# Kernel tuning notes

Hardware: AMD Instinct MI355X
Metric: run time of the kernel (lower is better)

The kernel has to match this reference:

```python
import jax, jax.numpy as jnp
import numpy as np

N, D, H, L = 100000, 128, 4, 2
C = D // H  # per-head channels
E = 1600000
NEG_SLOPE = 0.2
LN_EPS = 1e-5


def setup_inputs() -> dict:
    key = jax.random.key(0)
    ks = jax.random.split(key, 8)
    x = jax.random.normal(ks[0], (N, D), dtype=jnp.float32)
    edge_index = jax.random.randint(ks[1], (2, E), 0, N, dtype=jnp.int64)
    s = 1.0 / np.sqrt(D)
    Wl = jax.random.normal(ks[2], (L, D, D), dtype=jnp.float32) * s
    Wr = jax.random.normal(ks[3], (L, D, D), dtype=jnp.float32) * s
    att = jax.random.normal(ks[4], (L, H, C), dtype=jnp.float32) * (1.0 / np.sqrt(C))
    bias = jnp.zeros((L, D), dtype=jnp.float32)
    gamma = jnp.ones((L, D), dtype=jnp.float32)
    beta = jnp.zeros((L, D), dtype=jnp.float32)
    return {"x": x, "edge_index": edge_index, "Wl": Wl, "Wr": Wr,
            "att": att, "bias": bias, "gamma": gamma, "beta": beta}


def _gatv2_layer(h, src, dst, Wl, Wr, att, bias):
    # h: (N, D); src/dst: (E2,) with self-loops already appended
    xl = (h @ Wl).reshape(N, H, C)  # source-side transform
    xr = (h @ Wr).reshape(N, H, C)  # target-side transform
    e = jax.nn.leaky_relu(xl[src] + xr[dst], NEG_SLOPE)      # (E2, H, C)
    alpha = jnp.einsum('ehc,hc->eh', e, att)                 # (E2, H)
    # segment softmax over incoming edges of each destination node
    m = jax.ops.segment_max(alpha, dst, num_segments=N)      # (N, H)
    ea = jnp.exp(alpha - m[dst])
    s = jax.ops.segment_sum(ea, dst, num_segments=N)         # (N, H)
    a = ea / s[dst]                                          # (E2, H)
    out = jax.ops.segment_sum(a[:, :, None] * xl[src], dst, num_segments=N)
    return out.reshape(N, D) + bias


def _layer_norm(y, gamma, beta):
    mu = jnp.mean(y, axis=-1, keepdims=True)
    var = jnp.var(y, axis=-1, keepdims=True)
    return (y - mu) * jax.lax.rsqrt(var + LN_EPS) * gamma + beta


def reference(x, edge_index, Wl, Wr, att, bias, gamma, beta):
    # PyG GATv2Conv defaults: add_self_loops=True (eval mode: dropouts identity)
    loops = jnp.arange(N, dtype=edge_index.dtype)
    src = jnp.concatenate([edge_index[0], loops])
    dst = jnp.concatenate([edge_index[1], loops])
    h = x
    for l in range(L):
        g = _gatv2_layer(h, src, dst, Wl[l], Wr[l], att[l], bias[l])
        h = h + jax.nn.elu(_layer_norm(g, gamma[l], beta[l]))
    return h
```

## Files before the change

### kernel.cpp

```cpp
#include <hip/hip_runtime.h>
#include <hip/hip_fp16.h>
#include <math.h>

#define N_NODES 100000
#define D_FEAT  128
#define E_EDGES 1600000
#define E2      (E_EDGES + N_NODES)
#define NEG_SLOPE 0.2f
#define LN_EPS    1e-5f

#define NB   391
#define TS   8192
#define NTIL ((E2 + TS - 1) / TS)

typedef __attribute__((ext_vector_type(4))) float floatx4;
typedef _Float16 h2 __attribute__((ext_vector_type(2)));
typedef _Float16 h8 __attribute__((ext_vector_type(8)));

static __device__ __forceinline__ float fdot2f(h2 a, h2 b, float c) {
#if __has_builtin(__builtin_amdgcn_fdot2)
    return __builtin_amdgcn_fdot2(a, b, c, false);
#else
    return (float)a[0] * (float)b[0] + (float)a[1] * (float)b[1] + c;
#endif
}

static __device__ __forceinline__ h2 shfl_xor_h2(h2 v, int off) {
    int i = __builtin_bit_cast(int, v);
    i = __shfl_xor(i, off);
    return __builtin_bit_cast(h2, i);
}

__global__ __launch_bounds__(1024) void tile_count(const int* __restrict__ edge_dst,
                                                   int* __restrict__ tcnt) {
    __shared__ int h[NB];
    const int t = threadIdx.x;
    if (t < NB) h[t] = 0;
    __syncthreads();
    const int base = blockIdx.x * TS;
#pragma unroll
    for (int j = 0; j < TS / 1024; ++j) {
        int i = base + j * 1024 + t;
        if (i < E2) {
            int d = (i < E_EDGES) ? edge_dst[i] : (i - E_EDGES);
            atomicAdd(&h[d >> 8], 1);
        }
    }
    __syncthreads();
    if (t < NB) tcnt[blockIdx.x * NB + t] = h[t];
}

__global__ __launch_bounds__(256) void col_scan(const int* __restrict__ tcnt,
                                                int* __restrict__ toff,
                                                int* __restrict__ bcnt) {
    __shared__ int s[256];
    const int b = blockIdx.x;
    const int t = threadIdx.x;
    int v = (t < NTIL) ? tcnt[t * NB + b] : 0;
    s[t] = v;
    __syncthreads();
    for (int off = 1; off < 256; off <<= 1) {
        int x = (t >= off) ? s[t - off] : 0;
        __syncthreads();
        s[t] += x;
        __syncthreads();
    }
    if (t < NTIL) toff[t * NB + b] = s[t] - v;
    if (t == 255) bcnt[b] = s[255];
}

__global__ __launch_bounds__(512) void bucket_scan(const int* __restrict__ bcnt,
                                                   int* __restrict__ bstart,
                                                   int* __restrict__ rowstart) {
    __shared__ int s[512];
    const int t = threadIdx.x;
    int v = (t < NB) ? bcnt[t] : 0;
    s[t] = v;
    __syncthreads();
    for (int off = 1; off < 512; off <<= 1) {
        int x = (t >= off) ? s[t - off] : 0;
        __syncthreads();
        s[t] += x;
        __syncthreads();
    }
    if (t <= NB) bstart[t] = s[t] - v;
    if (t == 0) rowstart[N_NODES] = E2;
}

__global__ __launch_bounds__(1024) void tile_scatter(const int* __restrict__ edge_src,
                                                     const int* __restrict__ edge_dst,
                                                     const int* __restrict__ bstart,
                                                     const int* __restrict__ toff,
                                                     unsigned* __restrict__ pairbuf) {
    __shared__ int base[NB];
    __shared__ int cur[NB];
    const int t = threadIdx.x;
    if (t < NB) { base[t] = bstart[t] + toff[blockIdx.x * NB + t]; cur[t] = 0; }
    __syncthreads();
    const int tb = blockIdx.x * TS;
#pragma unroll
    for (int j = 0; j < TS / 1024; ++j) {
        int i = tb + j * 1024 + t;
        if (i < E2) {
            int d, sr;
            if (i < E_EDGES) { d = edge_dst[i]; sr = edge_src[i]; }
            else             { d = i - E_EDGES; sr = d; }
            int b = d >> 8;
            int rank = atomicAdd(&cur[b], 1);
            pairbuf[base[b] + rank] = (unsigned)sr | ((unsigned)(d & 255) << 17);
        }
    }
}

__global__ __launch_bounds__(1024) void bucketize(const unsigned* __restrict__ pairbuf,
                                                  const int* __restrict__ bstart,
                                                  int* __restrict__ rowstart,
                                                  int* __restrict__ csr_src) {
    __shared__ int cnt[256], sc[256], cur[256];
    const int blk = blockIdx.x;
    const int t = threadIdx.x;
    const int nbase = blk << 8;
    if (t < 256) cnt[t] = 0;
    __syncthreads();
    const int e0 = bstart[blk], e1 = bstart[blk + 1];
    for (int p = e0 + t; p < e1; p += 1024)
        atomicAdd(&cnt[pairbuf[p] >> 17], 1);
    __syncthreads();
    int v = (t < 256) ? cnt[t] : 0;
    if (t < 256) sc[t] = v;
    __syncthreads();
    for (int off = 1; off < 256; off <<= 1) {
        int x = (t < 256 && t >= off) ? sc[t - off] : 0;
        __syncthreads();
        if (t < 256) sc[t] += x;
        __syncthreads();
    }
    if (t < 256) {
        int excl = sc[t] - v;
        int node = nbase + t;
        if (node < N_NODES) rowstart[node] = e0 + excl;
        cur[t] = e0 + excl;
    }
    __syncthreads();
    for (int p = e0 + t; p < e1; p += 1024) {
        unsigned pr = pairbuf[p];
        int pos = atomicAdd(&cur[pr >> 17], 1);
        csr_src[pos] = (int)(pr & 0x1FFFF);
    }
}

__global__ void prep_wt(const float* __restrict__ Wl, const float* __restrict__ Wr,
                        const float* __restrict__ att,
                        _Float16* __restrict__ Wt, _Float16* __restrict__ atth) {
    int idx = blockIdx.x * 256 + threadIdx.x;
    if (idx < 65536) {
        int l    = idx >> 15;
        int rem  = idx & 32767;
        int side = rem >> 14;
        int cw   = rem & 16383;
        int col  = cw >> 7, k = cw & 127;
        const float* W = side ? Wr : Wl;
        Wt[idx] = (_Float16)W[l * 16384 + k * 128 + col];
    } else if (idx < 65536 + 256) {
        int j = idx - 65536;
        atth[j] = (_Float16)att[j];
    }
}

__global__ __launch_bounds__(256) void gemm_mfma3(
        const _Float16* __restrict__ hA,
        const float* __restrict__ Afp,
        const _Float16* __restrict__ Wt,
        _Float16* __restrict__ xl, _Float16* __restrict__ xr, int n_rows) {
    const int wave = threadIdx.x >> 6;
    const int lane = threadIdx.x & 63;
    const int m = lane & 15;
    const int q = lane >> 4;
    const int r0 = (blockIdx.x * 4 + wave) * 32;

    int arow0 = r0 + m;        if (arow0 >= n_rows) arow0 = n_rows - 1;
    int arow1 = r0 + 16 + m;   if (arow1 >= n_rows) arow1 = n_rows - 1;

    floatx4 acc[2][2][8];
#pragma unroll
    for (int s = 0; s < 2; ++s)
#pragma unroll
        for (int rt = 0; rt < 2; ++rt)
#pragma unroll
            for (int ct = 0; ct < 8; ++ct) acc[s][rt][ct] = (floatx4){0.f,0.f,0.f,0.f};

#pragma unroll
    for (int ks = 0; ks < 4; ++ks) {
        const int k0 = ks * 32 + q * 8;
        h8 a0, a1;
        if (Afp) {
            float4 f0 = *(const float4*)(Afp + (size_t)arow0 * 128 + k0);
            float4 f1 = *(const float4*)(Afp + (size_t)arow0 * 128 + k0 + 4);
            float4 g0 = *(const float4*)(Afp + (size_t)arow1 * 128 + k0);
            float4 g1 = *(const float4*)(Afp + (size_t)arow1 * 128 + k0 + 4);
            a0 = (h8){(_Float16)f0.x, (_Float16)f0.y, (_Float16)f0.z, (_Float16)f0.w,
                      (_Float16)f1.x, (_Float16)f1.y, (_Float16)f1.z, (_Float16)f1.w};
            a1 = (h8){(_Float16)g0.x, (_Float16)g0.y, (_Float16)g0.z, (_Float16)g0.w,
                      (_Float16)g1.x, (_Float16)g1.y, (_Float16)g1.z, (_Float16)g1.w};
        } else {
            a0 = *(const h8*)(hA + (size_t)arow0 * 128 + k0);
            a1 = *(const h8*)(hA + (size_t)arow1 * 128 + k0);
        }
#pragma unroll
        for (int s = 0; s < 2; ++s) {
#pragma unroll
            for (int ct = 0; ct < 8; ++ct) {
                h8 b = *(const h8*)(Wt + (size_t)s * 16384
                                    + (size_t)(ct * 16 + m) * 128 + k0);
                acc[s][0][ct] = __builtin_amdgcn_mfma_f32_16x16x32_f16(a0, b, acc[s][0][ct], 0, 0, 0);
                acc[s][1][ct] = __builtin_amdgcn_mfma_f32_16x16x32_f16(a1, b, acc[s][1][ct], 0, 0, 0);
            }
        }
    }

#pragma unroll
    for (int s = 0; s < 2; ++s) {
        _Float16* out = s ? xr : xl;
#pragma unroll
        for (int rt = 0; rt < 2; ++rt)
#pragma unroll
            for (int ct = 0; ct < 8; ++ct)
#pragma unroll
                for (int i = 0; i < 4; ++i) {
                    int row = r0 + rt * 16 + q * 4 + i;
                    if (row < n_rows)
                        out[(size_t)row * 128 + ct * 16 + m] = (_Float16)acc[s][rt][ct][i];
                }
    }
}

union U16 { uint4 u; h2 h[4]; };

__global__ __launch_bounds__(256) void gat_node10(
        const _Float16* __restrict__ xl,
        const _Float16* __restrict__ xr,
        const float* __restrict__ h_in_f32,
        const _Float16* __restrict__ h_in_f16,
        const int* __restrict__ rowstart, const int* __restrict__ csr_src,
        const _Float16* __restrict__ atth, const float* __restrict__ bias,
        const float* __restrict__ gamma, const float* __restrict__ beta,
        float* __restrict__ out_f32,
        _Float16* __restrict__ out_f16) {
    const int wave = threadIdx.x >> 6;
    const int lane = threadIdx.x & 63;
    const int node = blockIdx.x * 4 + wave;
    const int esub = lane >> 3;
    const int r    = lane & 7;
    const int c0   = r * 16;
    const int c    = c0 + 2 * esub;

    const int p0 = rowstart[node], p1 = rowstart[node + 1];
    const int pe = p1 - 1;

    U16 xra, xrb, ata, atb;
    {
        const uint4* xp = (const uint4*)(xr + (size_t)node * 128 + c0);
        xra.u = xp[0]; xrb.u = xp[1];
        const uint4* ap = (const uint4*)(atth + c0);
        ata.u = ap[0]; atb.u = ap[1];
    }
    const float2 bi = *(const float2*)(bias + c);
    const h2 ns2 = {(_Float16)NEG_SLOPE, (_Float16)NEG_SLOPE};

    const unsigned short* xls = (const unsigned short*)xl;

    float s = 0.f;
    h2 acc2[8];
#pragma unroll
    for (int j = 0; j < 8; ++j) acc2[j] = (h2){(_Float16)0.f, (_Float16)0.f};

    auto consume = [&](const U16& u0, const U16& u1, bool v) {
        float da = 0.f, db = 0.f;
#pragma unroll
        for (int qq = 0; qq < 4; ++qq) {
            h2 z  = u0.h[qq] + xra.h[qq];
            h2 lk = __builtin_elementwise_max(z, z * ns2);
            da = fdot2f(lk, ata.h[qq], da);
        }
#pragma unroll
        for (int qq = 0; qq < 4; ++qq) {
            h2 z  = u1.h[qq] + xrb.h[qq];
            h2 lk = __builtin_elementwise_max(z, z * ns2);
            db = fdot2f(lk, atb.h[qq], db);
        }
        float d = da + db;
        float alpha = d + __shfl_xor(d, 1);
        float w = v ? __expf(alpha) : 0.f;
        s += w;
        h2 w2 = {(_Float16)w, (_Float16)w};
#pragma unroll
        for (int qq = 0; qq < 4; ++qq)
            acc2[qq] = w2 * u0.h[qq] + acc2[qq];
#pragma unroll
        for (int qq = 0; qq < 4; ++qq)
            acc2[qq + 4] = w2 * u1.h[qq] + acc2[qq + 4];
    };

    int pA = p0 + esub;        if (pA > pe) pA = pe;
    int pB = p0 + 8 + esub;    if (pB > pe) pB = pe;
    int pC = p0 + 16 + esub;   if (pC > pe) pC = pe;
    int i0 = csr_src[pA];
    int i1 = csr_src[pB];
    int i2 = csr_src[pC];

    U16 s0a, s0b, s1a, s1b, s2a, s2b;
    { const uint4* rp = (const uint4*)(xls + (size_t)i0 * 128 + c0); s0a.u = rp[0]; s0b.u = rp[1]; }
    { const uint4* rp = (const uint4*)(xls + (size_t)i1 * 128 + c0); s1a.u = rp[0]; s1b.u = rp[1]; }

    int pb = p0;
    for (;;) {
        {
            int pn = pb + 24 + esub; if (pn > pe) pn = pe;
            int inew = csr_src[pn];
            if (pb + 16 < p1) {
                const uint4* rp = (const uint4*)(xls + (size_t)i2 * 128 + c0);
                s2a.u = rp[0]; s2b.u = rp[1];
            }
            consume(s0a, s0b, (pb + esub) < p1);
            i0 = inew;
            pb += 8; if (pb >= p1) break;
        }
        {
            int pn = pb + 24 + esub; if (pn > pe) pn = pe;
            int inew = csr_src[pn];
            if (pb + 16 < p1) {
                const uint4* rp = (const uint4*)(xls + (size_t)i0 * 128 + c0);
                s0a.u = rp[0]; s0b.u = rp[1];
            }
            consume(s1a, s1b, (pb + esub) < p1);
            i1 = inew;
            pb += 8; if (pb >= p1) break;
        }
        {
            int pn = pb + 24 + esub; if (pn > pe) pn = pe;
            int inew = csr_src[pn];
            if (pb + 16 < p1) {
                const uint4* rp = (const uint4*)(xls + (size_t)i1 * 128 + c0);
                s1a.u = rp[0]; s1b.u = rp[1];
            }
            consume(s2a, s2b, (pb + esub) < p1);
            i2 = inew;
            pb += 8; if (pb >= p1) break;
        }
    }

    float ssum = s;
    ssum += __shfl_xor(ssum, 8);
    ssum += __shfl_xor(ssum, 16);
    ssum += __shfl_xor(ssum, 32);

    const bool sel0 = (esub & 1) != 0;
    const bool sel1 = ((esub >> 1) & 1) != 0;
    const bool sel2 = ((esub >> 2) & 1) != 0;
    h2 b4[4];
#pragma unroll
    for (int k = 0; k < 4; ++k) {
        h2 keep = sel0 ? acc2[2 * k + 1] : acc2[2 * k];
        h2 send = sel0 ? acc2[2 * k]     : acc2[2 * k + 1];
        b4[k] = keep + shfl_xor_h2(send, 8);
    }
    h2 c2[2];
#pragma unroll
    for (int k = 0; k < 2; ++k) {
        h2 keep = sel1 ? b4[2 * k + 1] : b4[2 * k];
        h2 send = sel1 ? b4[2 * k]     : b4[2 * k + 1];
        c2[k] = keep + shfl_xor_h2(send, 16);
    }
    h2 keepf = sel2 ? c2[1] : c2[0];
    h2 sendf = sel2 ? c2[0] : c2[1];
    h2 tot = keepf + shfl_xor_h2(sendf, 32);

    const float invS = 1.f / ssum;
    float g0 = (float)tot[0] * invS + bi.x;
    float g1 = (float)tot[1] * invS + bi.y;

    const float2 ga = *(const float2*)(gamma + c);
    const float2 be = *(const float2*)(beta + c);
    float hx, hy;
    if (h_in_f16) {
        h2 hv = *(const h2*)(h_in_f16 + (size_t)node * 128 + c);
        hx = (float)hv[0]; hy = (float)hv[1];
    } else {
        float2 hv = *(const float2*)(h_in_f32 + (size_t)node * 128 + c);
        hx = hv.x; hy = hv.y;
    }

    float sum = g0 + g1, sq = g0 * g0 + g1 * g1;
#pragma unroll
    for (int off = 1; off < 64; off <<= 1) {
        sum += __shfl_xor(sum, off);
        sq  += __shfl_xor(sq, off);
    }
    float mu   = sum * (1.f / 128.f);
    float var  = sq * (1.f / 128.f) - mu * mu;
    float rstd = rsqrtf(var + LN_EPS);
    float y0 = (g0 - mu) * rstd * ga.x + be.x;
    float y1 = (g1 - mu) * rstd * ga.y + be.y;
    float e0 = (y0 > 0.f) ? y0 : (__expf(y0) - 1.f);
    float e1 = (y1 > 0.f) ? y1 : (__expf(y1) - 1.f);

    float ox = hx + e0;
    float oy = hy + e1;
    if (out_f32) {
        float2 o; o.x = ox; o.y = oy;
        *(float2*)(out_f32 + (size_t)node * 128 + c) = o;
    } else {
        h2 po = {(_Float16)ox, (_Float16)oy};
        *(h2*)(out_f16 + (size_t)node * 128 + c) = po;
    }
}

extern "C" void kernel_launch(void* const* d_in, const int* in_sizes, int n_in,
                              void* d_out, int out_size, void* d_ws, size_t ws_size,
                              hipStream_t stream) {
    const float* x     = (const float*)d_in[0];
    const int*   eidx  = (const int*)d_in[1];
    const float* Wl    = (const float*)d_in[2];
    const float* Wr    = (const float*)d_in[3];
    const float* att   = (const float*)d_in[4];
    const float* bias  = (const float*)d_in[5];
    const float* gamma = (const float*)d_in[6];
    const float* beta  = (const float*)d_in[7];
    float* out = (float*)d_out;

    char* ws = (char*)d_ws;
    _Float16* xl = (_Float16*)ws;              ws += (size_t)N_NODES * 128 * 2;
    _Float16* xr = (_Float16*)ws;              ws += (size_t)N_NODES * 128 * 2;
    _Float16* h16 = (_Float16*)ws;             ws += (size_t)N_NODES * 128 * 2;
    _Float16* Wt  = (_Float16*)ws;             ws += (size_t)65536 * 2;
    _Float16* atth = (_Float16*)ws;            ws += 256 * 2;
    unsigned* pairbuf = (unsigned*)ws;         ws += (size_t)E2 * 4;
    int* tcnt     = (int*)ws; ws += (size_t)NTIL * NB * 4;
    int* toff     = (int*)ws; ws += (size_t)NTIL * NB * 4;
    int* bcnt     = (int*)ws; ws += (NB + 1) * 4;
    int* bstart   = (int*)ws; ws += (NB + 1) * 4;
    int* rowstart = (int*)ws; ws += (size_t)(N_NODES + 4) * 4;
    int* csr_src  = (int*)ws; ws += (size_t)E2 * 4;

    const int* edge_src = eidx;
    const int* edge_dst = eidx + E_EDGES;

    prep_wt<<<257, 256, 0, stream>>>(Wl, Wr, att, Wt, atth);

    tile_count<<<NTIL, 1024, 0, stream>>>(edge_dst, tcnt);
    col_scan<<<NB, 256, 0, stream>>>(tcnt, toff, bcnt);
    bucket_scan<<<1, 512, 0, stream>>>(bcnt, bstart, rowstart);
    tile_scatter<<<NTIL, 1024, 0, stream>>>(edge_src, edge_dst, bstart, toff, pairbuf);
    bucketize<<<NB, 1024, 0, stream>>>(pairbuf, bstart, rowstart, csr_src);

    const int gemm_gx = (N_NODES + 127) / 128;
    for (int l = 0; l < 2; ++l) {
        gemm_mfma3<<<gemm_gx, 256, 0, stream>>>(
            (l == 0) ? nullptr : h16, (l == 0) ? x : nullptr,
            Wt + (size_t)l * 32768, xl, xr, N_NODES);
        gat_node10<<<N_NODES / 4, 256, 0, stream>>>(
            xl, xr,
            (l == 0) ? x : nullptr, (l == 0) ? nullptr : h16,
            rowstart, csr_src,
            atth + l * 128, bias + l * 128, gamma + l * 128, beta + l * 128,
            (l == 1) ? out : nullptr, (l == 0) ? h16 : nullptr);
    }
}
```

Baseline: 388.1 us.

## Replace two-level bucketed CSR build with global-atomic degree count and scatter

Replaces the tiled two-pass bucket sort (per-tile LDS histograms, column scans, pair buffer, per-bucket local sort) with a simple CSR build: global atomic degree count, a three-kernel prefix scan, and a scatter using per-node atomic cursors. This removes the intermediate pair buffer and its extra pass over the edges. In exchange it relies on 1.7M global atomics to random addresses, twice, and the order of edges within each row becomes nondeterministic.

```diff
diff --git a/kernel.cpp b/kernel.cpp
--- a/kernel.cpp
+++ b/kernel.cpp
@@ -9,10 +9,6 @@
 #define NEG_SLOPE 0.2f
 #define LN_EPS    1e-5f
 
-#define NB   391
-#define TS   8192
-#define NTIL ((E2 + TS - 1) / TS)
-
 typedef __attribute__((ext_vector_type(4))) float floatx4;
 typedef _Float16 h2 __attribute__((ext_vector_type(2)));
 typedef _Float16 h8 __attribute__((ext_vector_type(8)));
@@ -31,121 +27,81 @@
     return __builtin_bit_cast(h2, i);
 }
 
-__global__ __launch_bounds__(1024) void tile_count(const int* __restrict__ edge_dst,
-                                                   int* __restrict__ tcnt) {
-    __shared__ int h[NB];
+__global__ __launch_bounds__(1024) void zero_deg(int* __restrict__ deg) {
+    int i = blockIdx.x * 1024 + threadIdx.x;
+    if (i < N_NODES) deg[i] = 0;
+}
+
+__global__ __launch_bounds__(256) void count_deg(const int* __restrict__ edge_dst,
+                                                 int* __restrict__ deg) {
+    int i = blockIdx.x * 256 + threadIdx.x;
+    if (i < E2) {
+        int d = (i < E_EDGES) ? edge_dst[i] : (i - E_EDGES);
+        atomicAdd(&deg[d], 1);
+    }
+}
+
+__global__ __launch_bounds__(1024) void scan1(const int* __restrict__ deg,
+                                              int* __restrict__ rowstart,
+                                              int* __restrict__ btot) {
+    __shared__ int s[1024];
     const int t = threadIdx.x;
-    if (t < NB) h[t] = 0;
-    __syncthreads();
-    const int base = blockIdx.x * TS;
-#pragma unroll
-    for (int j = 0; j < TS / 1024; ++j) {
-        int i = base + j * 1024 + t;
-        if (i < E2) {
-            int d = (i < E_EDGES) ? edge_dst[i] : (i - E_EDGES);
-            atomicAdd(&h[d >> 8], 1);
-        }
-    }
-    __syncthreads();
-    if (t < NB) tcnt[blockIdx.x * NB + t] = h[t];
-}
-
-__global__ __launch_bounds__(256) void col_scan(const int* __restrict__ tcnt,
-                                                int* __restrict__ toff,
-                                                int* __restrict__ bcnt) {
-    __shared__ int s[256];
-    const int b = blockIdx.x;
-    const int t = threadIdx.x;
-    int v = (t < NTIL) ? tcnt[t * NB + b] : 0;
+    const int i = blockIdx.x * 1024 + t;
+    int v = (i < N_NODES) ? deg[i] : 0;
     s[t] = v;
     __syncthreads();
-    for (int off = 1; off < 256; off <<= 1) {
+    for (int off = 1; off < 1024; off <<= 1) {
         int x = (t >= off) ? s[t - off] : 0;
         __syncthreads();
         s[t] += x;
         __syncthreads();
     }
-    if (t < NTIL) toff[t * NB + b] = s[t] - v;
-    if (t == 255) bcnt[b] = s[255];
-}
-
-__global__ __launch_bounds__(512) void bucket_scan(const int* __restrict__ bcnt,
-                                                   int* __restrict__ bstart,
-                                                   int* __restrict__ rowstart) {
-    __shared__ int s[512];
+    if (i < N_NODES) rowstart[i] = s[t] - v;
+    if (t == 1023) btot[blockIdx.x] = s[1023];
+}
+
+__global__ __launch_bounds__(128) void scan2(const int* __restrict__ btot,
+                                             int* __restrict__ boff) {
+    __shared__ int s[128];
     const int t = threadIdx.x;
-    int v = (t < NB) ? bcnt[t] : 0;
+    int v = (t < 98) ? btot[t] : 0;
     s[t] = v;
     __syncthreads();
-    for (int off = 1; off < 512; off <<= 1) {
+    for (int off = 1; off < 128; off <<= 1) {
         int x = (t >= off) ? s[t - off] : 0;
         __syncthreads();
         s[t] += x;
         __syncthreads();
     }
-    if (t <= NB) bstart[t] = s[t] - v;
-    if (t == 0) rowstart[N_NODES] = E2;
-}
-
-__global__ __launch_bounds__(1024) void tile_scatter(const int* __restrict__ edge_src,
-                                                     const int* __restrict__ edge_dst,
-                                                     const int* __restrict__ bstart,
-                                                     const int* __restrict__ toff,
-                                                     unsigned* __restrict__ pairbuf) {
-    __shared__ int base[NB];
-    __shared__ int cur[NB];
+    boff[t] = s[t] - v;
+}
+
+__global__ __launch_bounds__(1024) void scan3(const int* __restrict__ boff,
+                                              int* __restrict__ rowstart,
+                                              int* __restrict__ cursor) {
     const int t = threadIdx.x;
-    if (t < NB) { base[t] = bstart[t] + toff[blockIdx.x * NB + t]; cur[t] = 0; }
-    __syncthreads();
-    const int tb = blockIdx.x * TS;
-#pragma unroll
-    for (int j = 0; j < TS / 1024; ++j) {
-        int i = tb + j * 1024 + t;
-        if (i < E2) {
-            int d, sr;
-            if (i < E_EDGES) { d = edge_dst[i]; sr = edge_src[i]; }
-            else             { d = i - E_EDGES; sr = d; }
-            int b = d >> 8;
-            int rank = atomicAdd(&cur[b], 1);
-            pairbuf[base[b] + rank] = (unsigned)sr | ((unsigned)(d & 255) << 17);
-        }
-    }
-}
-
-__global__ __launch_bounds__(1024) void bucketize(const unsigned* __restrict__ pairbuf,
-                                                  const int* __restrict__ bstart,
-                                                  int* __restrict__ rowstart,
-                                                  int* __restrict__ csr_src) {
-    __shared__ int cnt[256], sc[256], cur[256];
-    const int blk = blockIdx.x;
-    const int t = threadIdx.x;
-    const int nbase = blk << 8;
-    if (t < 256) cnt[t] = 0;
-    __syncthreads();
-    const int e0 = bstart[blk], e1 = bstart[blk + 1];
-    for (int p = e0 + t; p < e1; p += 1024)
-        atomicAdd(&cnt[pairbuf[p] >> 17], 1);
-    __syncthreads();
-    int v = (t < 256) ? cnt[t] : 0;
-    if (t < 256) sc[t] = v;
-    __syncthreads();
-    for (int off = 1; off < 256; off <<= 1) {
-        int x = (t < 256 && t >= off) ? sc[t - off] : 0;
-        __syncthreads();
-        if (t < 256) sc[t] += x;
-        __syncthreads();
-    }
-    if (t < 256) {
-        int excl = sc[t] - v;
-        int node = nbase + t;
-        if (node < N_NODES) rowstart[node] = e0 + excl;
-        cur[t] = e0 + excl;
-    }
-    __syncthreads();
-    for (int p = e0 + t; p < e1; p += 1024) {
-        unsigned pr = pairbuf[p];
-        int pos = atomicAdd(&cur[pr >> 17], 1);
-        csr_src[pos] = (int)(pr & 0x1FFFF);
+    const int b = blockIdx.x;
+    const int i = b * 1024 + t;
+    if (i < N_NODES) {
+        int v = rowstart[i] + boff[b];
+        rowstart[i] = v;
+        cursor[i] = v;
+    } else if (i == N_NODES) {
+        rowstart[N_NODES] = E2;
+    }
+}
+
+__global__ __launch_bounds__(256) void csr_scatter(const int* __restrict__ edge_src,
+                                                   const int* __restrict__ edge_dst,
+                                                   int* __restrict__ cursor,
+                                                   int* __restrict__ csr_src) {
+    int i = blockIdx.x * 256 + threadIdx.x;
+    if (i < E2) {
+        int d, sr;
+        if (i < E_EDGES) { d = edge_dst[i]; sr = edge_src[i]; }
+        else             { d = i - E_EDGES; sr = d; }
+        int pos = atomicAdd(&cursor[d], 1);
+        csr_src[pos] = sr;
     }
 }
 
@@ -434,12 +390,11 @@
     _Float16* h16 = (_Float16*)ws;             ws += (size_t)N_NODES * 128 * 2;
     _Float16* Wt  = (_Float16*)ws;             ws += (size_t)65536 * 2;
     _Float16* atth = (_Float16*)ws;            ws += 256 * 2;
-    unsigned* pairbuf = (unsigned*)ws;         ws += (size_t)E2 * 4;
-    int* tcnt     = (int*)ws; ws += (size_t)NTIL * NB * 4;
-    int* toff     = (int*)ws; ws += (size_t)NTIL * NB * 4;
-    int* bcnt     = (int*)ws; ws += (NB + 1) * 4;
-    int* bstart   = (int*)ws; ws += (NB + 1) * 4;
+    int* deg      = (int*)ws; ws += (size_t)(N_NODES + 4) * 4;
+    int* cursor   = (int*)ws; ws += (size_t)(N_NODES + 4) * 4;
     int* rowstart = (int*)ws; ws += (size_t)(N_NODES + 4) * 4;
+    int* btot     = (int*)ws; ws += 256 * 4;
+    int* boff     = (int*)ws; ws += 256 * 4;
     int* csr_src  = (int*)ws; ws += (size_t)E2 * 4;
 
     const int* edge_src = eidx;
@@ -447,11 +402,14 @@
 
     prep_wt<<<257, 256, 0, stream>>>(Wl, Wr, att, Wt, atth);
 
-    tile_count<<<NTIL, 1024, 0, stream>>>(edge_dst, tcnt);
-    col_scan<<<NB, 256, 0, stream>>>(tcnt, toff, bcnt);
-    bucket_scan<<<1, 512, 0, stream>>>(bcnt, bstart, rowstart);
-    tile_scatter<<<NTIL, 1024, 0, stream>>>(edge_src, edge_dst, bstart, toff, pairbuf);
-    bucketize<<<NB, 1024, 0, stream>>>(pairbuf, bstart, rowstart, csr_src);
+    const int nblk_n = (N_NODES + 1023) / 1024;
+    const int nblk_e = (E2 + 255) / 256;
+    zero_deg<<<nblk_n, 1024, 0, stream>>>(deg);
+    count_deg<<<nblk_e, 256, 0, stream>>>(edge_dst, deg);
+    scan1<<<nblk_n, 1024, 0, stream>>>(deg, rowstart, btot);
+    scan2<<<1, 128, 0, stream>>>(btot, boff);
+    scan3<<<nblk_n + 1, 1024, 0, stream>>>(boff, rowstart, cursor);
+    csr_scatter<<<nblk_e, 256, 0, stream>>>(edge_src, edge_dst, cursor, csr_src);
 
     const int gemm_gx = (N_NODES + 127) / 128;
     for (int l = 0; l < 2; ++l) {
```

After: 542.3 us. 1.4x slower.
